# Performance work log

Hardware: AMD Instinct MI355X
Metric: run time of the kernel (lower is better)

The kernel has to match this reference:

```python
import jax, jax.numpy as jnp
import numpy as np
import math

B, IN_DIM, HID, OUT_DIM = 8192, 64, 256, 4096
N_STEPS = 20


def logx_and_kl(loga, logb, alpha):
    # logx = log(alpha*a + (1-alpha)*b); kl = KL(x || b)
    logx = jnp.logaddexp(loga + jnp.log(alpha), logb + jnp.log(1.0 - alpha))
    kl = jnp.sum(jnp.exp(logx) * (logx - logb), axis=-1, keepdims=True)
    return logx, kl


def dkl_dalpha(loga, logb, logx):
    a_minus_b = jnp.exp(loga) - jnp.exp(logb)
    return jnp.sum(a_minus_b * (logx - logb + 1.0), axis=-1, keepdims=True)


def findalphafork(loga, logb, k, n_steps=N_STEPS):
    def body(i, carry):
        alpha, bot, top = carry
        logx, kl = logx_and_kl(loga, logb, alpha)
        bot = jnp.where(k >= kl, alpha, bot)
        top = jnp.where(k <= kl, alpha, top)
        d = dkl_dalpha(loga, logb, logx)
        delta = (k - kl) / (d + 1e-12)
        alpha = jnp.clip(alpha + delta,
                         bot * (15.0 / 16.0) + top * (1.0 / 16.0),
                         bot * 0.5 + top * 0.5)
        return alpha, bot, top

    init = (jnp.ones_like(k), jnp.zeros_like(k), jnp.ones_like(k))
    alpha, _, _ = jax.lax.fori_loop(0, n_steps, body, init)
    return alpha


def kl_fixed_mixture(k, loga, logb):
    alpha = findalphafork(loga, logb, k)
    return logx_and_kl(loga, logb, alpha)


def setup_inputs() -> dict:
    key = jax.random.key(0)
    ks = jax.random.split(key, 10)
    x = jax.random.normal(ks[0], (B, IN_DIM), dtype=jnp.float32)
    kl_budget = jax.random.uniform(ks[1], (B, 1), dtype=jnp.float32)
    log_base_dist = jax.nn.log_softmax(
        jax.random.normal(ks[2], (B, OUT_DIM), dtype=jnp.float32), axis=-1)
    W0 = jax.random.normal(ks[3], (HID, IN_DIM + 1), dtype=jnp.float32) * (0.05 / math.sqrt(IN_DIM + 1))
    b0 = jax.random.normal(ks[4], (HID,), dtype=jnp.float32) * 0.01
    W1 = jax.random.normal(ks[5], (HID, HID), dtype=jnp.float32) * (1.0 / math.sqrt(HID))
    b1 = jax.random.normal(ks[6], (HID,), dtype=jnp.float32) * 0.01
    W2 = jax.random.normal(ks[7], (OUT_DIM + 1, HID), dtype=jnp.float32) * 0.01
    b2 = jax.random.normal(ks[8], (OUT_DIM + 1,), dtype=jnp.float32) * 0.01
    return {"x": x, "kl_budget": kl_budget, "log_base_dist": log_base_dist,
            "W0": W0, "b0": b0, "W1": W1, "b1": b1, "W2": W2, "b2": b2,
            "actions_left": 16}


def reference(x, kl_budget, log_base_dist, W0, b0, W1, b1, W2, b2, actions_left):
    h = jnp.concatenate([x, kl_budget], axis=-1)  # [B, IN_DIM+1]
    for i, (W, b) in enumerate(((W0, b0), (W1, b1), (W2, b2))):
        if i != 0:
            h = jnp.tanh(h)
        h = h @ W.T + b
    # n_versions_last_layer == 1 -> selected_x = h
    kl_target = jax.nn.sigmoid(h[:, :1] - math.log(actions_left)) * kl_budget + 1e-6
    loga = h[:, 1:] + log_base_dist
    loga = loga - jnp.max(loga, axis=-1, keepdims=True)
    loga = loga - jax.nn.logsumexp(loga, axis=-1, keepdims=True)
    logx, kl_achieved = kl_fixed_mixture(kl_target, loga, log_base_dist)
    return jax.nn.softmax(logx, axis=-1), jnp.square(kl_achieved - kl_target)
```

## Files before the change

### kernel.cpp

```cpp
#include <hip/hip_runtime.h>
#include <hip/hip_bf16.h>
#include <math.h>

typedef float f32x4 __attribute__((ext_vector_type(4)));
typedef __bf16 bf16x8 __attribute__((ext_vector_type(8)));
typedef unsigned short ushort;

#define NROWS 8192
#define HID 256
#define NCOL 4096
#define NSTEPS 20

static __device__ inline float bf2f(ushort u) {
    union { unsigned int i; float f; } c; c.i = ((unsigned int)u) << 16; return c.f;
}
static __device__ inline ushort f2bf(float x) {
    __hip_bfloat16 h = __float2bfloat16(x);
    union { __hip_bfloat16 h; ushort u; } c; c.h = h; return c.u;
}
static __device__ inline void gload_lds16(const void* g, void* l) {
    __builtin_amdgcn_global_load_lds(
        (const __attribute__((address_space(1))) void*)g,
        (__attribute__((address_space(3))) void*)l, 16, 0, 0);
}

__global__ __launch_bounds__(256) void mlp01_kernel(
    const float* __restrict__ x, const float* __restrict__ klb,
    const float* __restrict__ W0, const float* __restrict__ b0,
    const float* __restrict__ W1, const float* __restrict__ b1,
    const float* __restrict__ W2, const float* __restrict__ b2,
    const int* __restrict__ AL,
    ushort* __restrict__ t_ext, float* __restrict__ kt)
{
    __shared__ float xk[8][66];
    __shared__ float h0[8][HID];
    __shared__ float ktred[8][4];
    const int tid = threadIdx.x;
    const int lane = tid & 63, w = tid >> 6;
    const int r0 = blockIdx.x * 8;

    for (int f = tid; f < 8 * 64; f += 256) {
        int r = f >> 6, k = f & 63;
        xk[r][k] = x[(r0 + r) * 64 + k];
    }
    if (tid < 8) xk[tid][64] = klb[r0 + tid];
    __syncthreads();

    {
        float acc[8];
        float bb = b0[tid];
        #pragma unroll
        for (int r = 0; r < 8; r++) acc[r] = bb;
        for (int k = 0; k < 65; k++) {
            float w0 = W0[tid * 65 + k];
            #pragma unroll
            for (int r = 0; r < 8; r++) acc[r] += w0 * xk[r][k];
        }
        #pragma unroll
        for (int r = 0; r < 8; r++) h0[r][tid] = tanhf(acc[r]);
    }
    __syncthreads();
    {
        float acc[8];
        float bb = b1[tid];
        #pragma unroll
        for (int r = 0; r < 8; r++) acc[r] = bb;
        for (int k = 0; k < HID; k++) {
            float w1 = W1[tid * HID + k];
            #pragma unroll
            for (int r = 0; r < 8; r++) acc[r] += w1 * h0[r][k];
        }
        const float w2v = W2[tid];
        __syncthreads();
        #pragma unroll
        for (int r = 0; r < 8; r++) {
            float v = tanhf(acc[r]);
            ushort hi = f2bf(v);
            float lo = v - bf2f(hi);
            size_t base = (size_t)(r0 + r) * 512;
            t_ext[base + tid] = hi;
            t_ext[base + 256 + tid] = f2bf(lo);
            float p = v * w2v;
            #pragma unroll
            for (int off = 1; off < 64; off <<= 1) p += __shfl_xor(p, off);
            if (lane == 0) ktred[r][w] = p;
        }
        __syncthreads();
        if (tid < 8) {
            float accv = ktred[tid][0] + ktred[tid][1] + ktred[tid][2] + ktred[tid][3];
            float z = accv + b2[0] - logf((float)AL[0]);
            float sg = 1.0f / (1.0f + expf(-z));
            kt[r0 + tid] = sg * klb[r0 + tid] + 1e-6f;
        }
    }
}

__global__ __launch_bounds__(256) void w2ext_kernel(const float* __restrict__ W2,
                                                    ushort* __restrict__ Bext)
{
    const int r = blockIdx.x, t = threadIdx.x;
    float v = W2[(size_t)(r + 1) * 256 + t];
    ushort hi = f2bf(v);
    float lo = v - bf2f(hi);
    Bext[(size_t)r * 512 + t] = hi;
    Bext[(size_t)r * 512 + 256 + t] = f2bf(lo);
}

__global__ __launch_bounds__(256) void gemm2_mfma(
    const ushort* __restrict__ Aext, const ushort* __restrict__ Bext,
    const float* __restrict__ b2, float* __restrict__ h2out)
{
    __shared__ ushort As[128 * 64];
    __shared__ ushort Bs[128 * 64];
    const int tid = threadIdx.x;
    const int lane = tid & 63, w = tid >> 6;
    const int m0 = blockIdx.y * 128, c0 = blockIdx.x * 128;
    const int wm = w & 1, wn = w >> 1;

    f32x4 acc[4][4];
    #pragma unroll
    for (int i = 0; i < 4; i++)
        #pragma unroll
        for (int j = 0; j < 4; j++) acc[i][j] = (f32x4){0.f, 0.f, 0.f, 0.f};

    int sg_row[4], sg_c[4];
    #pragma unroll
    for (int s = 0; s < 4; s++) {
        int idx = (s * 4 + w) * 512 + lane * 8;
        int row = idx >> 6;
        int cp = (idx >> 3) & 7;
        sg_row[s] = row;
        sg_c[s] = cp ^ (row & 7);
    }

    for (int kt = 0; kt < 8; kt++) {
        const int k0 = kt * 64;
        #pragma unroll
        for (int s = 0; s < 4; s++) {
            gload_lds16(&Aext[(size_t)(m0 + sg_row[s]) * 512 + k0 + sg_c[s] * 8],
                        &As[(s * 4 + w) * 512]);
            gload_lds16(&Bext[(size_t)(c0 + sg_row[s]) * 512 + k0 + sg_c[s] * 8],
                        &Bs[(s * 4 + w) * 512]);
        }
        __syncthreads();
        #pragma unroll
        for (int kk = 0; kk < 2; kk++) {
            const int cA = kk * 4 + (lane >> 4);
            bf16x8 af[4], bfr[4];
            #pragma unroll
            for (int i = 0; i < 4; i++) {
                int mr = wm * 64 + i * 16 + (lane & 15);
                af[i] = *(const bf16x8*)&As[mr * 64 + ((cA ^ (mr & 7)) * 8)];
                int nr = wn * 64 + i * 16 + (lane & 15);
                bfr[i] = *(const bf16x8*)&Bs[nr * 64 + ((cA ^ (nr & 7)) * 8)];
            }
            #pragma unroll
            for (int i = 0; i < 4; i++)
                #pragma unroll
                for (int j = 0; j < 4; j++)
                    acc[i][j] = __builtin_amdgcn_mfma_f32_16x16x32_bf16(
                        af[i], bfr[j], acc[i][j], 0, 0, 0);
        }
        __syncthreads();
    }

    const int colb = c0 + wn * 64 + (lane & 15);
    #pragma unroll
    for (int j = 0; j < 4; j++) {
        float bias = b2[1 + colb + j * 16];
        #pragma unroll
        for (int i = 0; i < 4; i++) {
            int rr = m0 + wm * 64 + i * 16 + (lane >> 4) * 4;
            #pragma unroll
            for (int q = 0; q < 4; q++)
                h2out[(size_t)(rr + q) * 4096 + colb + j * 16] = acc[i][j][q] + bias;
        }
    }
}

__global__ __launch_bounds__(256) void solve_kernel(
    float* __restrict__ outbuf, const float* __restrict__ logb_g,
    const float* __restrict__ ktarr)
{
    __shared__ float red[16];
    const int tid = threadIdx.x;
    const int lane = tid & 63, w = tid >> 6;

    for (int rr = 0; rr < 4; rr++) {
        const int r = blockIdx.x * 4 + rr;

        float amb[16];
        float eb[16];

        const float* rowA = outbuf + (size_t)r * 4096;
        const float* rowB = logb_g + (size_t)r * 4096;

        float s = 0.0f, t1 = 0.0f, c2 = 0.0f, seb = 0.0f;
        #pragma unroll
        for (int c = 0; c < 4; c++) {
            f32x4 av = *(const f32x4*)&rowA[c * 1024 + tid * 4];
            f32x4 bv = *(const f32x4*)&rowB[c * 1024 + tid * 4];
            #pragma unroll
            for (int j = 0; j < 4; j++) {
                int m = c * 4 + j;
                float e = __expf(av[j] + bv[j]);
                float b = __expf(bv[j]);
                amb[m] = e;
                eb[m] = b;
                s += e;
                t1 = fmaf(e, bv[j], t1);
                c2 = fmaf(b, bv[j], c2);
                seb += b;
            }
        }
        #pragma unroll
        for (int off = 1; off < 64; off <<= 1) {
            s   += __shfl_xor(s, off);
            t1  += __shfl_xor(t1, off);
            c2  += __shfl_xor(c2, off);
            seb += __shfl_xor(seb, off);
        }
        __syncthreads();
        if (lane == 0) {
            red[w * 4 + 0] = s;  red[w * 4 + 1] = t1;
            red[w * 4 + 2] = c2; red[w * 4 + 3] = seb;
        }
        __syncthreads();
        s   = red[0] + red[4] + red[8]  + red[12];
        t1  = red[1] + red[5] + red[9]  + red[13];
        c2  = red[2] + red[6] + red[10] + red[14];
        seb = red[3] + red[7] + red[11] + red[15];

        const float inv = 1.0f / s;
        const float C2 = c2;
        const float C3 = fmaf(inv, t1, -c2);
        const float C4 = (1.0f - seb) - C3;
        #pragma unroll
        for (int m = 0; m < 16; m++)
            amb[m] = fmaf(amb[m], inv, -eb[m]);

        const float k = ktarr[r];
        float alpha = 1.0f, bot = 0.0f, top = 1.0f;
        float a_eval = -1.0f, skl = 0.0f;

        for (int it = 0; it < NSTEPS; it++) {
            a_eval = alpha;
            float kacc = 0.0f, dacc = 0.0f;
            #pragma unroll
            for (int m = 0; m < 16; m++) {
                float xv = fmaf(alpha, amb[m], eb[m]);
                float lx = __logf(xv);
                kacc = fmaf(xv, lx, kacc);
                dacc = fmaf(amb[m], lx, dacc);
            }
            #pragma unroll
            for (int off = 1; off < 64; off <<= 1) {
                kacc += __shfl_xor(kacc, off);
                dacc += __shfl_xor(dacc, off);
            }
            __syncthreads();
            if (lane == 0) { red[w * 2 + 0] = kacc; red[w * 2 + 1] = dacc; }
            __syncthreads();
            kacc = red[0] + red[2] + red[4] + red[6];
            dacc = red[1] + red[3] + red[5] + red[7];

            float klc = kacc - C2 - alpha * C3;
            float dc  = dacc + C4;
            skl = klc;

            bot = (k >= klc) ? alpha : bot;
            top = (k <= klc) ? alpha : top;
            float delta = (k - klc) / (dc + 1e-12f);
            float lo = bot * (15.0f / 16.0f) + top * (1.0f / 16.0f);
            float hi = 0.5f * (bot + top);
            alpha = fminf(hi, fmaxf(lo, alpha + delta));
            if (top - bot < 1e-6f) break;
        }

        if (alpha != a_eval) {
            float kacc = 0.0f;
            #pragma unroll
            for (int m = 0; m < 16; m++) {
                float xv = fmaf(alpha, amb[m], eb[m]);
                kacc = fmaf(xv, __logf(xv), kacc);
            }
            #pragma unroll
            for (int off = 1; off < 64; off <<= 1) kacc += __shfl_xor(kacc, off);
            __syncthreads();
            if (lane == 0) red[w] = kacc;
            __syncthreads();
            kacc = red[0] + red[1] + red[2] + red[3];
            skl = kacc - C2 - alpha * C3;
        }

        const float spx = fmaf(alpha, 1.0f - seb, seb);
        const float invs = 1.0f / spx;

        float* orow = outbuf + (size_t)r * 4096;
        #pragma unroll
        for (int c = 0; c < 4; c++) {
            f32x4 o;
            #pragma unroll
            for (int j = 0; j < 4; j++)
                o[j] = fmaf(alpha, amb[c * 4 + j], eb[c * 4 + j]) * invs;
            *(f32x4*)&orow[c * 1024 + tid * 4] = o;
        }
        if (tid == 0) {
            float d = skl - k;
            outbuf[(size_t)NROWS * NCOL + r] = d * d;
        }
    }
}

extern "C" void kernel_launch(void* const* d_in, const int* in_sizes, int n_in,
                              void* d_out, int out_size, void* d_ws, size_t ws_size,
                              hipStream_t stream)
{
    const float* x    = (const float*)d_in[0];
    const float* klb  = (const float*)d_in[1];
    const float* logb = (const float*)d_in[2];
    const float* W0   = (const float*)d_in[3];
    const float* b0   = (const float*)d_in[4];
    const float* W1   = (const float*)d_in[5];
    const float* b1   = (const float*)d_in[6];
    const float* W2   = (const float*)d_in[7];
    const float* b2   = (const float*)d_in[8];
    const int*   AL   = (const int*)d_in[9];
    float* out = (float*)d_out;

    ushort* tws  = (ushort*)d_ws;
    ushort* Bext = tws + (size_t)8192 * 512;
    float*  kt   = (float*)(Bext + (size_t)4096 * 512);

    hipLaunchKernelGGL(mlp01_kernel, dim3(1024), dim3(256), 0, stream,
                       x, klb, W0, b0, W1, b1, W2, b2, AL, tws, kt);
    hipLaunchKernelGGL(w2ext_kernel, dim3(4096), dim3(256), 0, stream, W2, Bext);
    hipLaunchKernelGGL(gemm2_mfma, dim3(32, 64), dim3(256), 0, stream, tws, Bext, b2, out);
    hipLaunchKernelGGL(solve_kernel, dim3(2048), dim3(256), 0, stream, out, logb, kt);
}
```

Baseline: 183.0 us.

## Early-exit solve when alpha=1 satisfies budget, one row per block

The solve kernel now computes the KL at alpha=1 analytically from the softmax sums and writes the plain softmax straight away when the target budget is met, which skips computing exp(logb) and the whole Newton/bisection loop for those rows. Otherwise it reuses the alpha=1 evaluation as the first iteration, seeding alpha with a clamped Newton step. The grid changes from 4 rows per block to one row per block so early-exit rows free their CU slots independently. This adds a branch and divergence between blocks, and first-step results may differ slightly from the reference loop.

```diff
diff --git a/kernel.cpp b/kernel.cpp
--- a/kernel.cpp
+++ b/kernel.cpp
@@ -185,130 +185,169 @@
     __shared__ float red[16];
     const int tid = threadIdx.x;
     const int lane = tid & 63, w = tid >> 6;
-
-    for (int rr = 0; rr < 4; rr++) {
-        const int r = blockIdx.x * 4 + rr;
-
-        float amb[16];
-        float eb[16];
-
-        const float* rowA = outbuf + (size_t)r * 4096;
-        const float* rowB = logb_g + (size_t)r * 4096;
-
-        float s = 0.0f, t1 = 0.0f, c2 = 0.0f, seb = 0.0f;
-        #pragma unroll
-        for (int c = 0; c < 4; c++) {
-            f32x4 av = *(const f32x4*)&rowA[c * 1024 + tid * 4];
-            f32x4 bv = *(const f32x4*)&rowB[c * 1024 + tid * 4];
-            #pragma unroll
-            for (int j = 0; j < 4; j++) {
-                int m = c * 4 + j;
-                float e = __expf(av[j] + bv[j]);
-                float b = __expf(bv[j]);
-                amb[m] = e;
-                eb[m] = b;
-                s += e;
-                t1 = fmaf(e, bv[j], t1);
-                c2 = fmaf(b, bv[j], c2);
-                seb += b;
-            }
-        }
-        #pragma unroll
-        for (int off = 1; off < 64; off <<= 1) {
-            s   += __shfl_xor(s, off);
-            t1  += __shfl_xor(t1, off);
-            c2  += __shfl_xor(c2, off);
-            seb += __shfl_xor(seb, off);
-        }
-        __syncthreads();
-        if (lane == 0) {
-            red[w * 4 + 0] = s;  red[w * 4 + 1] = t1;
-            red[w * 4 + 2] = c2; red[w * 4 + 3] = seb;
-        }
-        __syncthreads();
-        s   = red[0] + red[4] + red[8]  + red[12];
-        t1  = red[1] + red[5] + red[9]  + red[13];
-        c2  = red[2] + red[6] + red[10] + red[14];
-        seb = red[3] + red[7] + red[11] + red[15];
-
-        const float inv = 1.0f / s;
-        const float C2 = c2;
-        const float C3 = fmaf(inv, t1, -c2);
-        const float C4 = (1.0f - seb) - C3;
-        #pragma unroll
-        for (int m = 0; m < 16; m++)
-            amb[m] = fmaf(amb[m], inv, -eb[m]);
-
-        const float k = ktarr[r];
-        float alpha = 1.0f, bot = 0.0f, top = 1.0f;
-        float a_eval = -1.0f, skl = 0.0f;
-
-        for (int it = 0; it < NSTEPS; it++) {
-            a_eval = alpha;
-            float kacc = 0.0f, dacc = 0.0f;
-            #pragma unroll
-            for (int m = 0; m < 16; m++) {
-                float xv = fmaf(alpha, amb[m], eb[m]);
-                float lx = __logf(xv);
-                kacc = fmaf(xv, lx, kacc);
-                dacc = fmaf(amb[m], lx, dacc);
-            }
-            #pragma unroll
-            for (int off = 1; off < 64; off <<= 1) {
-                kacc += __shfl_xor(kacc, off);
-                dacc += __shfl_xor(dacc, off);
-            }
-            __syncthreads();
-            if (lane == 0) { red[w * 2 + 0] = kacc; red[w * 2 + 1] = dacc; }
-            __syncthreads();
-            kacc = red[0] + red[2] + red[4] + red[6];
-            dacc = red[1] + red[3] + red[5] + red[7];
-
-            float klc = kacc - C2 - alpha * C3;
-            float dc  = dacc + C4;
-            skl = klc;
-
-            bot = (k >= klc) ? alpha : bot;
-            top = (k <= klc) ? alpha : top;
-            float delta = (k - klc) / (dc + 1e-12f);
-            float lo = bot * (15.0f / 16.0f) + top * (1.0f / 16.0f);
-            float hi = 0.5f * (bot + top);
-            alpha = fminf(hi, fmaxf(lo, alpha + delta));
-            if (top - bot < 1e-6f) break;
-        }
-
-        if (alpha != a_eval) {
-            float kacc = 0.0f;
-            #pragma unroll
-            for (int m = 0; m < 16; m++) {
-                float xv = fmaf(alpha, amb[m], eb[m]);
-                kacc = fmaf(xv, __logf(xv), kacc);
-            }
-            #pragma unroll
-            for (int off = 1; off < 64; off <<= 1) kacc += __shfl_xor(kacc, off);
-            __syncthreads();
-            if (lane == 0) red[w] = kacc;
-            __syncthreads();
-            kacc = red[0] + red[1] + red[2] + red[3];
-            skl = kacc - C2 - alpha * C3;
-        }
-
-        const float spx = fmaf(alpha, 1.0f - seb, seb);
-        const float invs = 1.0f / spx;
-
-        float* orow = outbuf + (size_t)r * 4096;
+    const int r = blockIdx.x;
+
+    const float* rowA = outbuf + (size_t)r * 4096;
+    const float* rowB = logb_g + (size_t)r * 4096;
+
+    f32x4 av4[4], bv4[4];
+    #pragma unroll
+    for (int c = 0; c < 4; c++) {
+        av4[c] = *(const f32x4*)&rowA[c * 1024 + tid * 4];
+        bv4[c] = *(const f32x4*)&rowB[c * 1024 + tid * 4];
+    }
+
+    float e[16];
+    float s = 0.0f, sav = 0.0f;
+    #pragma unroll
+    for (int c = 0; c < 4; c++)
+        #pragma unroll
+        for (int j = 0; j < 4; j++) {
+            int m = c * 4 + j;
+            e[m] = __expf(av4[c][j] + bv4[c][j]);
+            s += e[m];
+            sav = fmaf(e[m], av4[c][j], sav);
+        }
+    #pragma unroll
+    for (int off = 1; off < 64; off <<= 1) {
+        s   += __shfl_xor(s, off);
+        sav += __shfl_xor(sav, off);
+    }
+    if (lane == 0) { red[w * 2] = s; red[w * 2 + 1] = sav; }
+    __syncthreads();
+    s   = red[0] + red[2] + red[4] + red[6];
+    sav = red[1] + red[3] + red[5] + red[7];
+
+    const float k = ktarr[r];
+    const float lns = __logf(s);
+    const float inv = 1.0f / s;
+    const float kl1 = fmaf(sav, inv, -lns);
+
+    float* orow = outbuf + (size_t)r * 4096;
+
+    if (k >= kl1) {
         #pragma unroll
         for (int c = 0; c < 4; c++) {
             f32x4 o;
             #pragma unroll
-            for (int j = 0; j < 4; j++)
-                o[j] = fmaf(alpha, amb[c * 4 + j], eb[c * 4 + j]) * invs;
+            for (int j = 0; j < 4; j++) o[j] = e[c * 4 + j] * inv;
             *(f32x4*)&orow[c * 1024 + tid * 4] = o;
         }
         if (tid == 0) {
-            float d = skl - k;
+            float d = kl1 - k;
             outbuf[(size_t)NROWS * NCOL + r] = d * d;
         }
+        return;
+    }
+
+    float eb[16];
+    float c2 = 0.0f, c3 = 0.0f, seb = 0.0f, samv = 0.0f;
+    #pragma unroll
+    for (int c = 0; c < 4; c++)
+        #pragma unroll
+        for (int j = 0; j < 4; j++) {
+            int m = c * 4 + j;
+            float b = __expf(bv4[c][j]);
+            eb[m] = b;
+            float a = fmaf(e[m], inv, -b);
+            e[m] = a;
+            c2  = fmaf(b, bv4[c][j], c2);
+            c3  = fmaf(a, bv4[c][j], c3);
+            seb += b;
+            samv = fmaf(a, av4[c][j], samv);
+        }
+    #pragma unroll
+    for (int off = 1; off < 64; off <<= 1) {
+        c2   += __shfl_xor(c2, off);
+        c3   += __shfl_xor(c3, off);
+        seb  += __shfl_xor(seb, off);
+        samv += __shfl_xor(samv, off);
+    }
+    __syncthreads();
+    if (lane == 0) {
+        red[w * 4 + 0] = c2;  red[w * 4 + 1] = c3;
+        red[w * 4 + 2] = seb; red[w * 4 + 3] = samv;
+    }
+    __syncthreads();
+    c2   = red[0] + red[4] + red[8]  + red[12];
+    c3   = red[1] + red[5] + red[9]  + red[13];
+    seb  = red[2] + red[6] + red[10] + red[14];
+    samv = red[3] + red[7] + red[11] + red[15];
+
+    const float C2 = c2;
+    const float C3 = c3;
+    const float C4 = (1.0f - seb) - C3;
+
+    float skl = kl1, a_eval = 1.0f;
+    float bot = 0.0f, top = 1.0f;
+    float d1 = samv - lns * (1.0f - seb) + C4;
+    float alpha = fminf(0.5f, fmaxf(1.0f / 16.0f,
+                        1.0f + (k - kl1) / (d1 + 1e-12f)));
+
+    for (int it = 1; it < NSTEPS; it++) {
+        a_eval = alpha;
+        float kacc = 0.0f, dacc = 0.0f;
+        #pragma unroll
+        for (int m = 0; m < 16; m++) {
+            float xv = fmaf(alpha, e[m], eb[m]);
+            float lx = __logf(xv);
+            kacc = fmaf(xv, lx, kacc);
+            dacc = fmaf(e[m], lx, dacc);
+        }
+        #pragma unroll
+        for (int off = 1; off < 64; off <<= 1) {
+            kacc += __shfl_xor(kacc, off);
+            dacc += __shfl_xor(dacc, off);
+        }
+        __syncthreads();
+        if (lane == 0) { red[w * 2 + 0] = kacc; red[w * 2 + 1] = dacc; }
+        __syncthreads();
+        kacc = red[0] + red[2] + red[4] + red[6];
+        dacc = red[1] + red[3] + red[5] + red[7];
+
+        float klc = kacc - C2 - alpha * C3;
+        float dc  = dacc + C4;
+        skl = klc;
+
+        bot = (k >= klc) ? alpha : bot;
+        top = (k <= klc) ? alpha : top;
+        float delta = (k - klc) / (dc + 1e-12f);
+        float lo = bot * (15.0f / 16.0f) + top * (1.0f / 16.0f);
+        float hi = 0.5f * (bot + top);
+        alpha = fminf(hi, fmaxf(lo, alpha + delta));
+        if (top - bot < 1e-6f) break;
+    }
+
+    if (alpha != a_eval) {
+        float kacc = 0.0f;
+        #pragma unroll
+        for (int m = 0; m < 16; m++) {
+            float xv = fmaf(alpha, e[m], eb[m]);
+            kacc = fmaf(xv, __logf(xv), kacc);
+        }
+        #pragma unroll
+        for (int off = 1; off < 64; off <<= 1) kacc += __shfl_xor(kacc, off);
+        __syncthreads();
+        if (lane == 0) red[w] = kacc;
+        __syncthreads();
+        kacc = red[0] + red[1] + red[2] + red[3];
+        skl = kacc - C2 - alpha * C3;
+    }
+
+    const float spx = fmaf(alpha, 1.0f - seb, seb);
+    const float invs = 1.0f / spx;
+
+    #pragma unroll
+    for (int c = 0; c < 4; c++) {
+        f32x4 o;
+        #pragma unroll
+        for (int j = 0; j < 4; j++)
+            o[j] = fmaf(alpha, e[c * 4 + j], eb[c * 4 + j]) * invs;
+        *(f32x4*)&orow[c * 1024 + tid * 4] = o;
+    }
+    if (tid == 0) {
+        float d = skl - k;
+        outbuf[(size_t)NROWS * NCOL + r] = d * d;
     }
 }
 
@@ -336,5 +375,5 @@
                        x, klb, W0, b0, W1, b1, W2, b2, AL, tws, kt);
     hipLaunchKernelGGL(w2ext_kernel, dim3(4096), dim3(256), 0, stream, W2, Bext);
     hipLaunchKernelGGL(gemm2_mfma, dim3(32, 64), dim3(256), 0, stream, tws, Bext, b2, out);
-    hipLaunchKernelGGL(solve_kernel, dim3(2048), dim3(256), 0, stream, out, logb, kt);
-}
+    hipLaunchKernelGGL(solve_kernel, dim3(8192), dim3(256), 0, stream, out, logb, kt);
+}
```

After: 181.9 us. About the same (-0.6%).
